# Kernel optimization log

Measured on AMD Instinct MI355X. Metric: run time of the kernel, lower is better.

## Reference

```python
import jax, jax.numpy as jnp
import numpy as np

B, N = 8, 2048
EPS = 0.01

def setup_inputs() -> dict:
    key = jax.random.key(0)
    k_w, k_p, k_t = jax.random.split(key, 3)
    # W[:, 1] is the adjacency channel; entries are 0/1 floats
    W = jax.random.randint(k_w, (B, 2, N, N), 0, 2).astype(jnp.float32)
    pred = jax.random.normal(k_p, (B, N), dtype=jnp.float32)
    tgt = jax.random.randint(k_t, (B, N), 0, 16)  # unused by the loss, kept for signature fidelity
    return {"W": W, "pred": pred, "tgt": tgt}

def reference(W, pred, tgt):
    # adjacency mask from channel 1: [B, N, N]
    adj = W[:, 1] == 1.0
    # pairwise |pred_i - pred_j| < eps: [B, N, N]
    close = jnp.abs(pred[:, :, None] - pred[:, None, :]) < EPS
    # count of conflicting (same-color) adjacent pairs, returned as shape (1,) like torch mark
    mark = jnp.sum(jnp.where(adj & close, 1.0, 0.0), dtype=jnp.float32)
    return mark.reshape(1)
```

## Files before the change

kernel.cpp:

```cpp
#include <hip/hip_runtime.h>

#define BB 8
#define NN 2048
#define EPS 0.01f
#define ROWS 16
#define BLOCKS_PER_B 128

__global__ __launch_bounds__(256) void coloring_loss_kernel(
    const float* __restrict__ W,
    const float* __restrict__ pred,
    float* __restrict__ out)
{
    __shared__ float s_partial[4];

    const int bid  = blockIdx.x;
    const int b    = bid >> 7;
    const int row0 = (bid & 127) * ROWS;
    const int t    = threadIdx.x;

    const float* predb = pred + (size_t)b * NN;

    const float4 pj0 = ((const float4*)predb)[t];
    const float4 pj1 = ((const float4*)predb)[t + 256];

    float pis[ROWS];
#pragma unroll
    for (int r = 0; r < ROWS; ++r) pis[r] = predb[row0 + r];

    const float* wbase = W + (((size_t)b * 2 + 1) * (size_t)NN + (size_t)row0) * (size_t)NN;

    int cnt = 0;
#pragma unroll
    for (int r = 0; r < ROWS; ++r) {
        const float4* w4 = (const float4*)(wbase + (size_t)r * NN);
        const float4 w0 = w4[t];
        const float4 w1 = w4[t + 256];
        const float pi = pis[r];
        cnt += (w0.x == 1.0f) && (fabsf(pi - pj0.x) < EPS);
        cnt += (w0.y == 1.0f) && (fabsf(pi - pj0.y) < EPS);
        cnt += (w0.z == 1.0f) && (fabsf(pi - pj0.z) < EPS);
        cnt += (w0.w == 1.0f) && (fabsf(pi - pj0.w) < EPS);
        cnt += (w1.x == 1.0f) && (fabsf(pi - pj1.x) < EPS);
        cnt += (w1.y == 1.0f) && (fabsf(pi - pj1.y) < EPS);
        cnt += (w1.z == 1.0f) && (fabsf(pi - pj1.z) < EPS);
        cnt += (w1.w == 1.0f) && (fabsf(pi - pj1.w) < EPS);
    }

#pragma unroll
    for (int off = 32; off > 0; off >>= 1)
        cnt += __shfl_down(cnt, off, 64);

    const int wave = t >> 6;
    const int lane = t & 63;
    if (lane == 0) s_partial[wave] = (float)cnt;
    __syncthreads();

    if (t == 0) {
        const float s = s_partial[0] + s_partial[1] + s_partial[2] + s_partial[3];
        atomicAdd(out, s);
    }
}

extern "C" void kernel_launch(void* const* d_in, const int* in_sizes, int n_in,
                              void* d_out, int out_size, void* d_ws, size_t ws_size,
                              hipStream_t stream) {
    const float* W    = (const float*)d_in[0];
    const float* pred = (const float*)d_in[1];
    float* out = (float*)d_out;

    hipMemsetAsync(out, 0, sizeof(float), stream);

    coloring_loss_kernel<<<BB * BLOCKS_PER_B, 256, 0, stream>>>(W, pred, out);
}
```

Before: 325.7 us.

## Replace global atomic and memset with two-stage partial-sum reduction, halve rows per block

Each block now writes its partial count to workspace instead of atomically adding to the output, and a second single-block kernel reduces the partials. This removes the memset launch and the contention from many blocks hitting one atomic address. Rows per block drop from 16 to 8 so twice as many blocks are launched, and launch bounds request higher occupancy. The cost is an extra kernel launch plus a dependency on the workspace buffer being large enough.

```diff
diff --git a/kernel.cpp b/kernel.cpp
--- a/kernel.cpp
+++ b/kernel.cpp
@@ -3,19 +3,20 @@
 #define BB 8
 #define NN 2048
 #define EPS 0.01f
-#define ROWS 16
-#define BLOCKS_PER_B 128
+#define ROWS 8
+#define BLOCKS_PER_B 256
+#define NBLK (BB * BLOCKS_PER_B)
 
-__global__ __launch_bounds__(256) void coloring_loss_kernel(
+__global__ __launch_bounds__(256, 4) void coloring_loss_stage1(
     const float* __restrict__ W,
     const float* __restrict__ pred,
-    float* __restrict__ out)
+    float* __restrict__ partial)
 {
     __shared__ float s_partial[4];
 
     const int bid  = blockIdx.x;
-    const int b    = bid >> 7;
-    const int row0 = (bid & 127) * ROWS;
+    const int b    = bid >> 8;
+    const int row0 = (bid & 255) * ROWS;
     const int t    = threadIdx.x;
 
     const float* predb = pred + (size_t)b * NN;
@@ -56,9 +57,33 @@
     __syncthreads();
 
     if (t == 0) {
-        const float s = s_partial[0] + s_partial[1] + s_partial[2] + s_partial[3];
-        atomicAdd(out, s);
+        partial[bid] = s_partial[0] + s_partial[1] + s_partial[2] + s_partial[3];
     }
+}
+
+__global__ __launch_bounds__(256) void coloring_loss_stage2(
+    const float* __restrict__ partial,
+    float* __restrict__ out)
+{
+    __shared__ float s_partial[4];
+    const int t = threadIdx.x;
+
+    float s = 0.0f;
+#pragma unroll
+    for (int k = 0; k < NBLK / 256; ++k)
+        s += partial[t + k * 256];
+
+#pragma unroll
+    for (int off = 32; off > 0; off >>= 1)
+        s += __shfl_down(s, off, 64);
+
+    const int wave = t >> 6;
+    const int lane = t & 63;
+    if (lane == 0) s_partial[wave] = s;
+    __syncthreads();
+
+    if (t == 0)
+        out[0] = s_partial[0] + s_partial[1] + s_partial[2] + s_partial[3];
 }
 
 extern "C" void kernel_launch(void* const* d_in, const int* in_sizes, int n_in,
@@ -66,9 +91,9 @@
                               hipStream_t stream) {
     const float* W    = (const float*)d_in[0];
     const float* pred = (const float*)d_in[1];
-    float* out = (float*)d_out;
+    float* out     = (float*)d_out;
+    float* partial = (float*)d_ws;
 
-    hipMemsetAsync(out, 0, sizeof(float), stream);
-
-    coloring_loss_kernel<<<BB * BLOCKS_PER_B, 256, 0, stream>>>(W, pred, out);
+    coloring_loss_stage1<<<NBLK, 256, 0, stream>>>(W, pred, partial);
+    coloring_loss_stage2<<<1, 256, 0, stream>>>(partial, out);
 }
```

Result: no change. 322.2 us (-1.1%).
